# Optimization experiments

Measured on AMD Instinct MI355X. Metric: run time of the kernel, lower is better.

## Reference

```python
import jax, jax.numpy as jnp
import numpy as np

# ---- constants baked into the module (buffers / init defaults) ----
SAMPLE_RATE = 44100
K = 1.0 / SAMPLE_RATE                    # time step
MAX_OM = 10000.0 * 2.0 * np.pi           # fmax * 2*pi
MIN_OM = 20.0 * 2.0 * np.pi
LX = 0.5
TAU0, TAU1 = 6.0, 1.0
LOSS_F1 = 500.0
_OM2 = 2.0 * np.pi * LOSS_F1
_DOMSQ = _OM2 ** 2                        # OmDamp1 = 0
ALPHA = np.float32(3.0 * np.log(10.0) / _DOMSQ * (_OM2 ** 2 / TAU0))
BETA = np.float32(3.0 * np.log(10.0) / _DOMSQ * (1.0 / TAU1 - 1.0 / TAU0))
M_MAX = N_MAX = 80
_gm, _gn = np.meshgrid(np.arange(1, M_MAX + 1), np.arange(1, N_MAX + 1), indexing='ij')
M_VEC = jnp.asarray(_gm.reshape(-1), dtype=jnp.float32)   # [6400]
N_VEC = jnp.asarray(_gn.reshape(-1), dtype=jnp.float32)   # [6400]


def setup_inputs() -> dict:
    z = jnp.zeros((), dtype=jnp.float32)
    return {
        'mu_raw': z, 'D_over_mu_raw': z, 'T0_over_mu_raw': z,
        'Ly_raw': z, 'xo_raw': z, 'yo_raw': z,
        'num_samples': 44100,  # duration=1.0 s
    }


def reference(mu_raw, D_over_mu_raw, T0_over_mu_raw, Ly_raw, xo_raw, yo_raw, num_samples):
    sp = jax.nn.softplus
    mu = sp(mu_raw) + 1e-4
    D_over_mu = sp(D_over_mu_raw) + 1e-4
    T0_over_mu = sp(T0_over_mu_raw) + 1e-4
    Ly = 1.1 + (4.0 - 1.1) * ((jnp.tanh(Ly_raw) + 1.0) / 2.0)
    xo = 0.49 * LX + (1.0 - 0.49) * LX * ((jnp.tanh(xo_raw) + 1.0) / 2.0)
    yo = 0.51 * Ly + (1.0 - 0.51) * Ly * ((jnp.tanh(yo_raw) + 1.0) / 2.0)
    xi = 0.1 * LX
    yi = 0.1 * Ly

    pi = np.float32(np.pi)
    g1 = (M_VEC * pi / LX) ** 2 + (N_VEC * pi / Ly) ** 2          # [6400]
    omega = jnp.sqrt(jax.nn.relu(T0_over_mu * g1 + D_over_mu * g1 * g1))
    valid = ((omega <= MAX_OM) & (omega >= MIN_OM)).astype(omega.dtype)

    in_w = jnp.cos(xi * pi * M_VEC / LX) * jnp.cos(yi * pi * N_VEC / Ly)
    out_w = jnp.cos(xo * pi * M_VEC / LX) * jnp.cos(yo * pi * N_VEC / Ly)
    sigma = ALPHA + BETA * omega ** 2
    ms = 0.25 * mu * LX * Ly
    P = out_w * in_w * (K ** 2) * jnp.exp(-sigma * K) / ms * valid  # [6400]

    n = jnp.arange(num_samples, dtype=jnp.float32)                # [N]
    # [6400, N] damped-sinusoid matrix, then reduce over modes
    decay_env = jnp.exp(-sigma[:, None] * (n[None, :] - 1.0) * K)
    sine = jnp.sin(n[None, :] * (omega[:, None] * K)) / (jnp.sin(omega * K) + 1e-8)[:, None]
    displacement = jnp.sum(P[:, None] * decay_env * sine, axis=0)  # [N]

    # normalize=True, velCalc=False (module defaults)
    peak = jnp.max(jnp.abs(displacement)) + 1e-8
    return displacement / peak
```

## Files before the change

### kernel.cpp

```cpp
#include <hip/hip_runtime.h>
#include <math.h>

#define BLK 256
#define G 16
#define NMODES 6400
#define STRIPE (NMODES / G)
#define MDIM 80

__device__ float4   g_records[NMODES];
__device__ unsigned g_maxbits;

__device__ __forceinline__ float v_fract(float x){ float r; asm("v_fract_f32 %0, %1" : "=v"(r) : "v"(x)); return r; }
__device__ __forceinline__ float v_sin_rev(float x){ float r; asm("v_sin_f32 %0, %1" : "=v"(r) : "v"(x)); return r; }
__device__ __forceinline__ float v_exp2(float x){ float r; asm("v_exp_f32 %0, %1" : "=v"(r) : "v"(x)); return r; }

__device__ __forceinline__ double softplus_d(double x) {
    return (x > 30.0) ? x : log1p(exp(x));
}

__global__ __launch_bounds__(BLK) void setup_zero_kernel(
    const float* __restrict__ mu_raw_p, const float* __restrict__ Dmu_raw_p,
    const float* __restrict__ T0mu_raw_p, const float* __restrict__ Ly_raw_p,
    const float* __restrict__ xo_raw_p, const float* __restrict__ yo_raw_p,
    float* __restrict__ out, int N)
{
    const int gid = blockIdx.x * BLK + threadIdx.x;
    if (gid < N) out[gid] = 0.0f;
    if (gid == 0) g_maxbits = 0u;
    if (gid >= NMODES) return;

    const double PI_D     = 3.14159265358979323846;
    const double TWO_PI_D = 6.28318530717958647693;
    const double INV2PI_D = 0.15915494309189533577;
    const double LOG2E_D  = 1.44269504088896340736;
    const double LX = 0.5;
    const double Kd = 1.0 / 44100.0;
    const double MAX_OM = 10000.0 * TWO_PI_D;
    const double MIN_OM = 20.0 * TWO_PI_D;

    const double OM2   = TWO_PI_D * 500.0;
    const double DOMSQ = OM2 * OM2;
    const float ALPHA_F = (float)(3.0 * log(10.0) / DOMSQ * (OM2 * OM2 / 6.0));
    const float BETA_F  = (float)(3.0 * log(10.0) / DOMSQ * (1.0 / 1.0 - 1.0 / 6.0));

    const double mu   = softplus_d((double)mu_raw_p[0])  + 1e-4;
    const double Dmu  = softplus_d((double)Dmu_raw_p[0]) + 1e-4;
    const double T0mu = softplus_d((double)T0mu_raw_p[0]) + 1e-4;
    const double Ly   = 1.1 + (4.0 - 1.1) * ((tanh((double)Ly_raw_p[0]) + 1.0) * 0.5);
    const double xo   = 0.49 * LX + (1.0 - 0.49) * LX * ((tanh((double)xo_raw_p[0]) + 1.0) * 0.5);
    const double yo   = 0.51 * Ly + (1.0 - 0.51) * Ly * ((tanh((double)yo_raw_p[0]) + 1.0) * 0.5);
    const double xi = 0.1 * LX;
    const double yi = 0.1 * Ly;
    const double ms = 0.25 * mu * LX * Ly;

    const double mm = (double)(gid / MDIM + 1);
    const double nn = (double)(gid % MDIM + 1);
    const double a1 = mm * PI_D / LX;
    const double a2 = nn * PI_D / Ly;
    const double g1 = a1 * a1 + a2 * a2;
    double osq = T0mu * g1 + Dmu * g1 * g1;
    if (osq < 0.0) osq = 0.0;
    const double omega = sqrt(osq);

    float4 rec = make_float4(0.0f, 0.0f, 0.0f, 0.0f);
    if (omega >= MIN_OM && omega <= MAX_OM) {
        const double w     = omega * Kd;
        const double sig   = (double)ALPHA_F + (double)BETA_F * (omega * omega);
        const double in_w  = cos(xi * a1) * cos(yi * a2);
        const double out_w = cos(xo * a1) * cos(yo * a2);
        const double denom = sin(w) + 1e-8;
        const double A = out_w * in_w * (Kd * Kd) / ms / denom;
        const double wrev = w * INV2PI_D;
        const float hi = (float)wrev;
        const float lo = (float)(wrev - (double)hi);
        rec = make_float4(hi, lo, (float)(-sig * Kd * LOG2E_D), (float)A);
    }
    g_records[gid] = rec;
}

__global__ __launch_bounds__(BLK, 8) void modal_main_kernel(
    float* __restrict__ out, int N)
{
    __shared__ float4 md[STRIPE];
    __shared__ int cnt;
    if (threadIdx.x == 0) cnt = 0;
    __syncthreads();

    const int n0  = blockIdx.x * BLK;
    const int gy  = blockIdx.y;
    const float n0f = (float)n0;
    const int lane = threadIdx.x & 63;

    for (int j0 = 0; j0 < STRIPE; j0 += BLK) {
        const int j = j0 + threadIdx.x;
        bool alive = false;
        float4 orec;
        if (j < STRIPE) {
            const float4 rec = g_records[gy + G * j];
            if (rec.w != 0.0f) {
                const float ampf = rec.w * v_exp2(rec.z * n0f);
                if (fabsf(ampf) >= 1e-18f) {
                    const double wrev = (double)rec.x + (double)rec.y;
                    const double p0   = (double)n0 * wrev;
                    const float base  = (float)(p0 - rint(p0));
                    orec = make_float4(base, rec.x, rec.z, ampf);
                    alive = true;
                }
            }
        }
        const unsigned long long mask = __ballot(alive);
        const int nw = __popcll(mask);
        int base_slot = 0;
        if (lane == 0 && nw) base_slot = atomicAdd(&cnt, nw);
        base_slot = __shfl(base_slot, 0, 64);
        if (alive) {
            const int s = base_slot + __popcll(mask & ((1ull << lane) - 1ull));
            md[s] = orec;
        }
    }
    __syncthreads();

    const int count = cnt;
    if (count == 0) return;
    const int n = n0 + threadIdx.x;
    if (n >= N) return;

    const float tf = (float)threadIdx.x;
    float acc = 0.0f;
    for (int j = 0; j < count; ++j) {
        const float4 v = md[j];
        const float rev = fmaf(tf, v.y, v.x);
        const float s   = v_sin_rev(v_fract(rev));
        const float e   = v_exp2(v.z * tf);
        acc = fmaf(v.w * e, s, acc);
    }
    if (acc != 0.0f) atomicAdd(&out[n], acc);
}

__global__ __launch_bounds__(BLK) void block_max_kernel(
    const float* __restrict__ out, int N)
{
    const int nvec = N >> 2;
    const int i = blockIdx.x * BLK + threadIdx.x;
    float m = 0.0f;
    if (i < nvec) {
        const float4 v = ((const float4*)out)[i];
        m = fmaxf(fmaxf(fabsf(v.x), fabsf(v.y)), fmaxf(fabsf(v.z), fabsf(v.w)));
    }
    if (blockIdx.x == 0 && threadIdx.x < (N & 3))
        m = fmaxf(m, fabsf(out[(nvec << 2) + threadIdx.x]));
    #pragma unroll
    for (int o = 32; o > 0; o >>= 1) m = fmaxf(m, __shfl_down(m, o));
    __shared__ float sm[4];
    const int w = threadIdx.x >> 6, l = threadIdx.x & 63;
    if (l == 0) sm[w] = m;
    __syncthreads();
    if (threadIdx.x == 0) {
        const float mm = fmaxf(fmaxf(sm[0], sm[1]), fmaxf(sm[2], sm[3]));
        atomicMax(&g_maxbits, __float_as_uint(mm));
    }
}

__global__ __launch_bounds__(BLK) void scale_kernel(float* __restrict__ out, int N)
{
    const float inv = 1.0f / (__uint_as_float(g_maxbits) + 1e-8f);
    const int nvec = N >> 2;
    const int i = blockIdx.x * BLK + threadIdx.x;
    if (i < nvec) {
        float4 v = ((float4*)out)[i];
        v.x *= inv; v.y *= inv; v.z *= inv; v.w *= inv;
        ((float4*)out)[i] = v;
    }
    if (blockIdx.x == 0 && threadIdx.x < (N & 3))
        out[(nvec << 2) + threadIdx.x] *= inv;
}

extern "C" void kernel_launch(void* const* d_in, const int* in_sizes, int n_in,
                              void* d_out, int out_size, void* d_ws, size_t ws_size,
                              hipStream_t stream) {
    const float* mu_raw   = (const float*)d_in[0];
    const float* Dmu_raw  = (const float*)d_in[1];
    const float* T0mu_raw = (const float*)d_in[2];
    const float* Ly_raw   = (const float*)d_in[3];
    const float* xo_raw   = (const float*)d_in[4];
    const float* yo_raw   = (const float*)d_in[5];
    float* out = (float*)d_out;
    const int N = out_size;
    int nb = (N + BLK - 1) / BLK;
    const int nb_setup = (NMODES + BLK - 1) / BLK;
    if (nb < nb_setup) nb = nb_setup;
    const int nbv = ((N >> 2) + BLK - 1) / BLK > 0 ? ((N >> 2) + BLK - 1) / BLK : 1;

    setup_zero_kernel<<<nb, BLK, 0, stream>>>(mu_raw, Dmu_raw, T0mu_raw,
                                              Ly_raw, xo_raw, yo_raw, out, N);
    modal_main_kernel<<<dim3((N + BLK - 1) / BLK, G), BLK, 0, stream>>>(out, N);
    block_max_kernel<<<nbv, BLK, 0, stream>>>(out, N);
    scale_kernel<<<nbv, BLK, 0, stream>>>(out, N);
}
```

Measured before the change: 96.14 us.

## Compute four samples per mode via angle-addition recurrence; replace atomics with partial buffers

Each thread now produces four output samples spaced 256 apart. It evaluates sin/cos once and advances the phase and decay with precomputed per-mode rotation (cos, sin of 256*w) and decay factors, which cuts transcendental work per sample. Per-group partial sums are written to a workspace buffer, and a combine kernel sums them and computes the max, replacing atomicAdd and the zeroing pass. The mode split doubles to 32 groups. The cost is recurrence rounding drift, a slightly looser amplitude cutoff, and extra workspace traffic.

```diff
diff --git a/kernel.cpp b/kernel.cpp
--- a/kernel.cpp
+++ b/kernel.cpp
@@ -2,30 +2,32 @@
 #include <math.h>
 
 #define BLK 256
-#define G 16
+#define G 32
 #define NMODES 6400
 #define STRIPE (NMODES / G)
 #define MDIM 80
-
-__device__ float4   g_records[NMODES];
+#define TILE 1024
+#define SPT 4
+
+__device__ float4   g_rec1[NMODES];
+__device__ float4   g_rec2[NMODES];
 __device__ unsigned g_maxbits;
 
 __device__ __forceinline__ float v_fract(float x){ float r; asm("v_fract_f32 %0, %1" : "=v"(r) : "v"(x)); return r; }
 __device__ __forceinline__ float v_sin_rev(float x){ float r; asm("v_sin_f32 %0, %1" : "=v"(r) : "v"(x)); return r; }
+__device__ __forceinline__ float v_cos_rev(float x){ float r; asm("v_cos_f32 %0, %1" : "=v"(r) : "v"(x)); return r; }
 __device__ __forceinline__ float v_exp2(float x){ float r; asm("v_exp_f32 %0, %1" : "=v"(r) : "v"(x)); return r; }
 
 __device__ __forceinline__ double softplus_d(double x) {
     return (x > 30.0) ? x : log1p(exp(x));
 }
 
-__global__ __launch_bounds__(BLK) void setup_zero_kernel(
+__global__ __launch_bounds__(BLK) void setup_kernel(
     const float* __restrict__ mu_raw_p, const float* __restrict__ Dmu_raw_p,
     const float* __restrict__ T0mu_raw_p, const float* __restrict__ Ly_raw_p,
-    const float* __restrict__ xo_raw_p, const float* __restrict__ yo_raw_p,
-    float* __restrict__ out, int N)
+    const float* __restrict__ xo_raw_p, const float* __restrict__ yo_raw_p)
 {
     const int gid = blockIdx.x * BLK + threadIdx.x;
-    if (gid < N) out[gid] = 0.0f;
     if (gid == 0) g_maxbits = 0u;
     if (gid >= NMODES) return;
 
@@ -62,7 +64,8 @@
     if (osq < 0.0) osq = 0.0;
     const double omega = sqrt(osq);
 
-    float4 rec = make_float4(0.0f, 0.0f, 0.0f, 0.0f);
+    float4 r1 = make_float4(0.0f, 0.0f, 0.0f, 0.0f);
+    float4 r2 = make_float4(1.0f, 0.0f, 1.0f, 0.0f);
     if (omega >= MIN_OM && omega <= MAX_OM) {
         const double w     = omega * Kd;
         const double sig   = (double)ALPHA_F + (double)BETA_F * (omega * omega);
@@ -73,37 +76,44 @@
         const double wrev = w * INV2PI_D;
         const float hi = (float)wrev;
         const float lo = (float)(wrev - (double)hi);
-        rec = make_float4(hi, lo, (float)(-sig * Kd * LOG2E_D), (float)A);
-    }
-    g_records[gid] = rec;
-}
-
-__global__ __launch_bounds__(BLK, 8) void modal_main_kernel(
-    float* __restrict__ out, int N)
-{
-    __shared__ float4 md[STRIPE];
+        const double z = -sig * Kd * LOG2E_D;
+        const double dph = 256.0 * w;
+        r1 = make_float4(hi, lo, (float)z, (float)A);
+        r2 = make_float4((float)cos(dph), (float)sin(dph),
+                         (float)exp2(256.0 * z), 0.0f);
+    }
+    g_rec1[gid] = r1;
+    g_rec2[gid] = r2;
+}
+
+__global__ __launch_bounds__(BLK) void modal_main_kernel(
+    float* __restrict__ partial, int pstride)
+{
+    __shared__ float4 md1[STRIPE];
+    __shared__ float4 md2[STRIPE];
     __shared__ int cnt;
     if (threadIdx.x == 0) cnt = 0;
     __syncthreads();
 
-    const int n0  = blockIdx.x * BLK;
+    const int n0  = blockIdx.x * TILE;
     const int gy  = blockIdx.y;
     const float n0f = (float)n0;
     const int lane = threadIdx.x & 63;
 
-    for (int j0 = 0; j0 < STRIPE; j0 += BLK) {
-        const int j = j0 + threadIdx.x;
+    {
+        const int j = threadIdx.x;
         bool alive = false;
-        float4 orec;
+        float4 o1, o2;
         if (j < STRIPE) {
-            const float4 rec = g_records[gy + G * j];
+            const float4 rec = g_rec1[gy + G * j];
             if (rec.w != 0.0f) {
-                const float ampf = rec.w * v_exp2(rec.z * n0f);
-                if (fabsf(ampf) >= 1e-18f) {
+                const float amp0 = rec.w * v_exp2(rec.z * n0f);
+                if (fabsf(amp0) >= 1e-20f) {
                     const double wrev = (double)rec.x + (double)rec.y;
                     const double p0   = (double)n0 * wrev;
                     const float base  = (float)(p0 - rint(p0));
-                    orec = make_float4(base, rec.x, rec.z, ampf);
+                    o1 = make_float4(base, rec.x, rec.z, amp0);
+                    o2 = g_rec2[gy + G * j];
                     alive = true;
                 }
             }
@@ -115,40 +125,70 @@
         base_slot = __shfl(base_slot, 0, 64);
         if (alive) {
             const int s = base_slot + __popcll(mask & ((1ull << lane) - 1ull));
-            md[s] = orec;
+            md1[s] = o1;
+            md2[s] = o2;
         }
     }
     __syncthreads();
 
     const int count = cnt;
-    if (count == 0) return;
-    const int n = n0 + threadIdx.x;
-    if (n >= N) return;
-
     const float tf = (float)threadIdx.x;
-    float acc = 0.0f;
+    float acc0 = 0.0f, acc1 = 0.0f, acc2 = 0.0f, acc3 = 0.0f;
     for (int j = 0; j < count; ++j) {
-        const float4 v = md[j];
-        const float rev = fmaf(tf, v.y, v.x);
-        const float s   = v_sin_rev(v_fract(rev));
-        const float e   = v_exp2(v.z * tf);
-        acc = fmaf(v.w * e, s, acc);
-    }
-    if (acc != 0.0f) atomicAdd(&out[n], acc);
-}
-
-__global__ __launch_bounds__(BLK) void block_max_kernel(
-    const float* __restrict__ out, int N)
+        const float4 v1 = md1[j];
+        const float4 v2 = md2[j];
+        const float rev = v_fract(fmaf(tf, v1.y, v1.x));
+        float s = v_sin_rev(rev);
+        float c = v_cos_rev(rev);
+        float amp = v1.w * v_exp2(v1.z * tf);
+        acc0 = fmaf(amp, s, acc0);
+        const float cD = v2.x, sD = v2.y, eD = v2.z;
+        float s1 = fmaf(s, cD,  c * sD);
+        float c1 = fmaf(c, cD, -s * sD);
+        amp *= eD;
+        acc1 = fmaf(amp, s1, acc1);
+        float s2 = fmaf(s1, cD,  c1 * sD);
+        float c2 = fmaf(c1, cD, -s1 * sD);
+        amp *= eD;
+        acc2 = fmaf(amp, s2, acc2);
+        float s3 = fmaf(s2, cD,  c2 * sD);
+        amp *= eD;
+        acc3 = fmaf(amp, s3, acc3);
+        (void)c2; (void)s3;
+    }
+    float* row = partial + (size_t)gy * pstride + n0 + threadIdx.x;
+    row[0]   = acc0;
+    row[256] = acc1;
+    row[512] = acc2;
+    row[768] = acc3;
+}
+
+__global__ __launch_bounds__(BLK) void combine_max_kernel(
+    const float* __restrict__ partial, int pstride,
+    float* __restrict__ out, int N)
 {
     const int nvec = N >> 2;
     const int i = blockIdx.x * BLK + threadIdx.x;
     float m = 0.0f;
     if (i < nvec) {
-        const float4 v = ((const float4*)out)[i];
-        m = fmaxf(fmaxf(fabsf(v.x), fabsf(v.y)), fmaxf(fabsf(v.z), fabsf(v.w)));
-    }
-    if (blockIdx.x == 0 && threadIdx.x < (N & 3))
-        m = fmaxf(m, fabsf(out[(nvec << 2) + threadIdx.x]));
+        float4 s = make_float4(0.0f, 0.0f, 0.0f, 0.0f);
+        const float4* p4 = (const float4*)partial;
+        const int vstride = pstride >> 2;
+        #pragma unroll
+        for (int g = 0; g < G; ++g) {
+            const float4 v = p4[(size_t)g * vstride + i];
+            s.x += v.x; s.y += v.y; s.z += v.z; s.w += v.w;
+        }
+        ((float4*)out)[i] = s;
+        m = fmaxf(fmaxf(fabsf(s.x), fabsf(s.y)), fmaxf(fabsf(s.z), fabsf(s.w)));
+    }
+    if (blockIdx.x == 0 && threadIdx.x < (N & 3)) {
+        const int n = (nvec << 2) + threadIdx.x;
+        float sv = 0.0f;
+        for (int g = 0; g < G; ++g) sv += partial[(size_t)g * pstride + n];
+        out[n] = sv;
+        m = fmaxf(m, fabsf(sv));
+    }
     #pragma unroll
     for (int o = 32; o > 0; o >>= 1) m = fmaxf(m, __shfl_down(m, o));
     __shared__ float sm[4];
@@ -185,15 +225,18 @@
     const float* xo_raw   = (const float*)d_in[4];
     const float* yo_raw   = (const float*)d_in[5];
     float* out = (float*)d_out;
+    float* partial = (float*)d_ws;
     const int N = out_size;
-    int nb = (N + BLK - 1) / BLK;
+
+    const int ntiles  = (N + TILE - 1) / TILE;
+    const int pstride = ntiles * TILE;
     const int nb_setup = (NMODES + BLK - 1) / BLK;
-    if (nb < nb_setup) nb = nb_setup;
-    const int nbv = ((N >> 2) + BLK - 1) / BLK > 0 ? ((N >> 2) + BLK - 1) / BLK : 1;
-
-    setup_zero_kernel<<<nb, BLK, 0, stream>>>(mu_raw, Dmu_raw, T0mu_raw,
-                                              Ly_raw, xo_raw, yo_raw, out, N);
-    modal_main_kernel<<<dim3((N + BLK - 1) / BLK, G), BLK, 0, stream>>>(out, N);
-    block_max_kernel<<<nbv, BLK, 0, stream>>>(out, N);
+    int nbv = ((N >> 2) + BLK - 1) / BLK;
+    if (nbv < 1) nbv = 1;
+
+    setup_kernel<<<nb_setup, BLK, 0, stream>>>(mu_raw, Dmu_raw, T0mu_raw,
+                                               Ly_raw, xo_raw, yo_raw);
+    modal_main_kernel<<<dim3(ntiles, G), BLK, 0, stream>>>(partial, pstride);
+    combine_max_kernel<<<nbv, BLK, 0, stream>>>(partial, pstride, out, N);
     scale_kernel<<<nbv, BLK, 0, stream>>>(out, N);
 }
```

New measurement: 92.35 us. 3.9% less time.
